# Kernel optimization log

Measured on AMD Instinct MI355X. Metric: run time of the kernel, lower is better.

The kernel has to match this reference:

```python
import jax, jax.numpy as jnp
import numpy as np

NUM_ENTITIES = 500000
NUM_RELATIONS = 1000
NUM_ENTITY_TYPES = 100
NUM_RELATION_TYPES = 50
D = 128
B = 16384


def setup_inputs() -> dict:
    key = jax.random.key(0)
    ks = jax.random.split(key, 9)
    u = lambda k, shape: jax.random.uniform(k, shape, jnp.float32, -0.1, 0.1)
    return {
        "heads": jax.random.randint(ks[0], (B,), 0, NUM_ENTITIES),
        "relations": jax.random.randint(ks[1], (B,), 0, NUM_RELATIONS),
        "tails": jax.random.randint(ks[2], (B,), 0, NUM_ENTITIES),
        "entity_types": jax.random.randint(ks[3], (B,), 0, NUM_ENTITY_TYPES),
        "relation_types": jax.random.randint(ks[4], (B,), 0, NUM_RELATION_TYPES),
        "entity_emb": u(ks[5], (NUM_ENTITIES, D)),
        "relation_emb": u(ks[6], (NUM_RELATIONS, D)),
        "entity_type_proj": u(ks[7], (NUM_ENTITY_TYPES, D * D)),
        "relation_type_proj": u(ks[8], (NUM_RELATION_TYPES, D * D)),
    }


def reference(heads, relations, tails, entity_types, relation_types,
              entity_emb, relation_emb, entity_type_proj, relation_type_proj):
    h = entity_emb[heads]                     # [B, D]
    r = relation_emb[relations]               # [B, D]
    t = entity_emb[tails]                     # [B, D]
    Pe = entity_type_proj[entity_types].reshape(-1, D, D)      # [B, D, D]
    Pr = relation_type_proj[relation_types].reshape(-1, D, D)  # [B, D, D]
    ph = jnp.einsum('bij,bj->bi', Pe, h)
    pt = jnp.einsum('bij,bj->bi', Pe, t)
    pr = jnp.einsum('bij,bj->bi', Pr, r)
    diff = ph + pr - pt                       # [B, D]
    return jnp.linalg.norm(diff, axis=1)      # [B]
```

## Files before the change

kernel.cpp:

```cpp
#include <hip/hip_runtime.h>
#include <math.h>

#define D 128
#define MTILE 32
#define MAXCH 1280
#define NB 1024

#define W_NCH   0
#define W_CHP0  16
#define W_CHN   (16 + MAXCH)
#define W_CHTT  (16 + 2 * MAXCH)
#define W_SRT   4096

__global__ __launch_bounds__(NB) void bucket_kernel(
    const int* __restrict__ etypes, const int* __restrict__ rtypes,
    int* __restrict__ ws, int B)
{
    __shared__ int cnt_e[128], cnt_r[64], off_e[128], off_r[64], tmp[128];
    __shared__ int s_nche;
    const int tid = threadIdx.x;

    if (tid < 128) cnt_e[tid] = 0;
    if (tid < 64)  cnt_r[tid] = 0;
    __syncthreads();
    for (int b = tid; b < B; b += NB) {
        atomicAdd(&cnt_e[etypes[b]], 1);
        atomicAdd(&cnt_r[rtypes[b]], 1);
    }
    __syncthreads();

    int c = (tid < 128) ? cnt_e[tid] : 0;
    if (tid < 128) tmp[tid] = c;
    __syncthreads();
    for (int off = 1; off < 128; off <<= 1) {
        int v = (tid < 128 && tid >= off) ? tmp[tid - off] : 0;
        __syncthreads();
        if (tid < 128) tmp[tid] += v;
        __syncthreads();
    }
    int excl = (tid < 128) ? (tmp[tid] - c) : 0;
    if (tid < 128) off_e[tid] = excl;
    int nch = (tid < 128) ? ((c + MTILE - 1) / MTILE) : 0;
    __syncthreads();
    if (tid < 128) tmp[tid] = nch;
    __syncthreads();
    for (int off = 1; off < 128; off <<= 1) {
        int v = (tid < 128 && tid >= off) ? tmp[tid - off] : 0;
        __syncthreads();
        if (tid < 128) tmp[tid] += v;
        __syncthreads();
    }
    if (tid < 128) {
        int cexcl = tmp[tid] - nch;
        for (int q = 0; q < nch; ++q) {
            int ci = cexcl + q;
            ws[W_CHP0 + ci] = excl + q * MTILE;
            int rem = c - q * MTILE;
            ws[W_CHN + ci] = rem < MTILE ? rem : MTILE;
            ws[W_CHTT + ci] = tid;
        }
    }
    if (tid == 127) s_nche = tmp[127];
    __syncthreads();
    const int NEch = s_nche;

    c = (tid < 64) ? cnt_r[tid] : 0;
    if (tid < 128) tmp[tid] = c;
    __syncthreads();
    for (int off = 1; off < 128; off <<= 1) {
        int v = (tid < 128 && tid >= off) ? tmp[tid - off] : 0;
        __syncthreads();
        if (tid < 128) tmp[tid] += v;
        __syncthreads();
    }
    excl = (tid < 128) ? (tmp[tid] - c) : 0;
    if (tid < 64) off_r[tid] = excl;
    nch = (tid < 64) ? ((c + MTILE - 1) / MTILE) : 0;
    __syncthreads();
    if (tid < 128) tmp[tid] = nch;
    __syncthreads();
    for (int off = 1; off < 128; off <<= 1) {
        int v = (tid < 128 && tid >= off) ? tmp[tid - off] : 0;
        __syncthreads();
        if (tid < 128) tmp[tid] += v;
        __syncthreads();
    }
    if (tid < 64) {
        int cexcl = tmp[tid] - nch;
        for (int q = 0; q < nch; ++q) {
            int ci = NEch + cexcl + q;
            ws[W_CHP0 + ci] = excl + q * MTILE;
            int rem = c - q * MTILE;
            ws[W_CHN + ci] = rem < MTILE ? rem : MTILE;
            ws[W_CHTT + ci] = tid | 256;
        }
    }
    if (tid == 127) ws[W_NCH] = NEch + tmp[127];
    __syncthreads();

    int* srt_e = ws + W_SRT;
    int* inv_e = srt_e + B;
    int* srt_r = inv_e + B;
    int* inv_r = srt_r + B;
    for (int b = tid; b < B; b += NB) {
        int pe = atomicAdd(&off_e[etypes[b]], 1);
        srt_e[pe] = b; inv_e[b] = pe;
        int pr = atomicAdd(&off_r[rtypes[b]], 1);
        srt_r[pr] = b; inv_r[b] = pr;
    }
}

__global__ __launch_bounds__(256) void gemm_fused(
    const int* __restrict__ heads, const int* __restrict__ tails,
    const int* __restrict__ rels,
    const float* __restrict__ eemb, const float* __restrict__ remb,
    const float* __restrict__ eproj, const float* __restrict__ rproj,
    const int* __restrict__ ws, int B,
    float* __restrict__ Ye, float* __restrict__ Yr)
{
    const int nch = ws[W_NCH];
    if ((int)blockIdx.x >= nch) return;
    const int p0  = ws[W_CHP0 + blockIdx.x];
    const int nr  = ws[W_CHN  + blockIdx.x];
    const int tts = ws[W_CHTT + blockIdx.x];
    const int side = tts >> 8, tt = tts & 255;
    const int* srt = ws + W_SRT + (side ? 2 * B : 0);
    const float* P = (side ? rproj : eproj) + (size_t)tt * D * D;
    float* Y = side ? Yr : Ye;

    __shared__ float Xs[MTILE * 132];
    __shared__ float Ps[D * 36];

    const int tid = threadIdx.x;

    for (int idx = tid; idx < MTILE * 32; idx += 256) {
        int row = idx >> 5, kq = idx & 31;
        float4 v = {0.f, 0.f, 0.f, 0.f};
        if (row < nr) {
            int b = srt[p0 + row];
            if (side == 0) {
                float4 hv = ((const float4*)(eemb + (size_t)heads[b] * D))[kq];
                float4 tv = ((const float4*)(eemb + (size_t)tails[b] * D))[kq];
                v.x = hv.x - tv.x; v.y = hv.y - tv.y;
                v.z = hv.z - tv.z; v.w = hv.w - tv.w;
            } else {
                v = ((const float4*)(remb + (size_t)rels[b] * D))[kq];
            }
        }
        *(float4*)&Xs[row * 132 + kq * 4] = v;
    }

    float acc[2][8];
    #pragma unroll
    for (int j = 0; j < 2; ++j)
        #pragma unroll
        for (int i = 0; i < 8; ++i) acc[j][i] = 0.f;

    const int ty = tid >> 4, tx = tid & 15;

    for (int k0 = 0; k0 < 32; k0 += 8) {
        __syncthreads();
        for (int idx = tid; idx < 1024; idx += 256) {
            int n = idx >> 3, kq = idx & 7;
            float4 v = *(const float4*)&P[(size_t)n * D + (k0 + kq) * 4];
            *(float4*)&Ps[n * 36 + kq * 4] = v;
        }
        __syncthreads();

        #pragma unroll
        for (int kq = 0; kq < 8; ++kq) {
            float4 xv[2], pv[8];
            #pragma unroll
            for (int j = 0; j < 2; ++j)
                xv[j] = *(const float4*)&Xs[(ty * 2 + j) * 132 + (k0 + kq) * 4];
            #pragma unroll
            for (int i = 0; i < 8; ++i)
                pv[i] = *(const float4*)&Ps[(i * 16 + tx) * 36 + kq * 4];
            #pragma unroll
            for (int j = 0; j < 2; ++j)
                #pragma unroll
                for (int i = 0; i < 8; ++i)
                    acc[j][i] += xv[j].x * pv[i].x + xv[j].y * pv[i].y
                               + xv[j].z * pv[i].z + xv[j].w * pv[i].w;
        }
    }

    #pragma unroll
    for (int j = 0; j < 2; ++j) {
        int m = ty * 2 + j;
        if (m < nr) {
            float* yp = Y + (size_t)(p0 + m) * D + tx;
            #pragma unroll
            for (int i = 0; i < 8; ++i) yp[i * 16] = acc[j][i];
        }
    }
}

__global__ __launch_bounds__(256) void norm_kernel(
    const int* __restrict__ ws, int B,
    const float* __restrict__ Ye, const float* __restrict__ Yr,
    float* __restrict__ out)
{
    int wave = threadIdx.x >> 6, lane = threadIdx.x & 63;
    int gb = blockIdx.x * 4 + wave;
    if (gb >= B) return;
    int re = ws[W_SRT + B + gb];
    int rr = ws[W_SRT + 3 * B + gb];
    float2 a = ((const float2*)(Ye + (size_t)re * D))[lane];
    float2 c = ((const float2*)(Yr + (size_t)rr * D))[lane];
    float x0 = a.x + c.x, x1 = a.y + c.y;
    float ss = x0 * x0 + x1 * x1;
    #pragma unroll
    for (int off = 32; off > 0; off >>= 1)
        ss += __shfl_down(ss, off, 64);
    if (lane == 0) out[gb] = sqrtf(ss);
}

extern "C" void kernel_launch(void* const* d_in, const int* in_sizes, int n_in,
                              void* d_out, int out_size, void* d_ws, size_t ws_size,
                              hipStream_t stream) {
    const int*   heads     = (const int*)d_in[0];
    const int*   relations = (const int*)d_in[1];
    const int*   tails     = (const int*)d_in[2];
    const int*   etypes    = (const int*)d_in[3];
    const int*   rtypes    = (const int*)d_in[4];
    const float* eemb      = (const float*)d_in[5];
    const float* remb      = (const float*)d_in[6];
    const float* eproj     = (const float*)d_in[7];
    const float* rproj     = (const float*)d_in[8];
    float* out = (float*)d_out;

    const int B = in_sizes[0];
    int* ws = (int*)d_ws;
    float* Ye = (float*)d_ws + (W_SRT + 4 * B);
    float* Yr = Ye + (size_t)B * D;

    bucket_kernel<<<1, NB, 0, stream>>>(etypes, rtypes, ws, B);
    gemm_fused<<<MAXCH, 256, 0, stream>>>(heads, tails, relations,
                                          eemb, remb, eproj, rproj, ws, B, Ye, Yr);
    norm_kernel<<<(B + 3) / 4, 256, 0, stream>>>(ws, B, Ye, Yr, out);
}
```

Measured before the change: 426.8 us.

## Split single-block bucketing into parallel count, scan, and scatter kernels

Replaces the one-block bucket sort with four kernels: zero the counters, count types with a grid-wide global atomic histogram, build offsets and chunk descriptors in one block using a single combined scan plus a binary search per chunk, and scatter indices with a grid-wide pass. This targets the serial cost of one 1024-thread block walking all 16384 items twice. In exchange it adds three kernel launches and contended global atomics on a small number of counters. The scatter order within a type is now nondeterministic across blocks, but the output does not depend on that order.

```diff
diff --git a/kernel.cpp b/kernel.cpp
--- a/kernel.cpp
+++ b/kernel.cpp
@@ -4,32 +4,44 @@
 #define D 128
 #define MTILE 32
 #define MAXCH 1280
-#define NB 1024
 
 #define W_NCH   0
-#define W_CHP0  16
-#define W_CHN   (16 + MAXCH)
-#define W_CHTT  (16 + 2 * MAXCH)
-#define W_SRT   4096
-
-__global__ __launch_bounds__(NB) void bucket_kernel(
+#define W_CNT_E 16
+#define W_CNT_R 144
+#define W_RUN_E 208
+#define W_RUN_R 336
+#define W_CHP0  512
+#define W_CHN   (512 + MAXCH)
+#define W_CHTT  (512 + 2 * MAXCH)
+#define W_SRT   8192
+
+__global__ __launch_bounds__(256) void zero_kernel(int* ws) {
+    int tid = threadIdx.x;
+    if (tid < 192) ws[W_CNT_E + tid] = 0;
+}
+
+__global__ __launch_bounds__(256) void count_kernel(
     const int* __restrict__ etypes, const int* __restrict__ rtypes,
     int* __restrict__ ws, int B)
 {
-    __shared__ int cnt_e[128], cnt_r[64], off_e[128], off_r[64], tmp[128];
-    __shared__ int s_nche;
+    int b = blockIdx.x * blockDim.x + threadIdx.x;
+    if (b < B) {
+        atomicAdd(&ws[W_CNT_E + etypes[b]], 1);
+        atomicAdd(&ws[W_CNT_R + rtypes[b]], 1);
+    }
+}
+
+__global__ __launch_bounds__(256) void scan_build_kernel(int* __restrict__ ws) {
+    __shared__ int s_cnt[192];
+    __shared__ int s_off[192];
+    __shared__ int s_cs[193];
+    __shared__ int tmp[256];
     const int tid = threadIdx.x;
 
-    if (tid < 128) cnt_e[tid] = 0;
-    if (tid < 64)  cnt_r[tid] = 0;
-    __syncthreads();
-    for (int b = tid; b < B; b += NB) {
-        atomicAdd(&cnt_e[etypes[b]], 1);
-        atomicAdd(&cnt_r[rtypes[b]], 1);
-    }
-    __syncthreads();
-
-    int c = (tid < 128) ? cnt_e[tid] : 0;
+    if (tid < 192) s_cnt[tid] = ws[W_CNT_E + tid];
+    __syncthreads();
+
+    int c = (tid < 128) ? s_cnt[tid] : 0;
     if (tid < 128) tmp[tid] = c;
     __syncthreads();
     for (int off = 1; off < 128; off <<= 1) {
@@ -38,74 +50,66 @@
         if (tid < 128) tmp[tid] += v;
         __syncthreads();
     }
-    int excl = (tid < 128) ? (tmp[tid] - c) : 0;
-    if (tid < 128) off_e[tid] = excl;
-    int nch = (tid < 128) ? ((c + MTILE - 1) / MTILE) : 0;
-    __syncthreads();
-    if (tid < 128) tmp[tid] = nch;
-    __syncthreads();
-    for (int off = 1; off < 128; off <<= 1) {
-        int v = (tid < 128 && tid >= off) ? tmp[tid - off] : 0;
-        __syncthreads();
-        if (tid < 128) tmp[tid] += v;
-        __syncthreads();
-    }
-    if (tid < 128) {
-        int cexcl = tmp[tid] - nch;
-        for (int q = 0; q < nch; ++q) {
-            int ci = cexcl + q;
-            ws[W_CHP0 + ci] = excl + q * MTILE;
-            int rem = c - q * MTILE;
-            ws[W_CHN + ci] = rem < MTILE ? rem : MTILE;
-            ws[W_CHTT + ci] = tid;
-        }
-    }
-    if (tid == 127) s_nche = tmp[127];
-    __syncthreads();
-    const int NEch = s_nche;
-
-    c = (tid < 64) ? cnt_r[tid] : 0;
-    if (tid < 128) tmp[tid] = c;
-    __syncthreads();
-    for (int off = 1; off < 128; off <<= 1) {
-        int v = (tid < 128 && tid >= off) ? tmp[tid - off] : 0;
-        __syncthreads();
-        if (tid < 128) tmp[tid] += v;
-        __syncthreads();
-    }
-    excl = (tid < 128) ? (tmp[tid] - c) : 0;
-    if (tid < 64) off_r[tid] = excl;
-    nch = (tid < 64) ? ((c + MTILE - 1) / MTILE) : 0;
-    __syncthreads();
-    if (tid < 128) tmp[tid] = nch;
-    __syncthreads();
-    for (int off = 1; off < 128; off <<= 1) {
-        int v = (tid < 128 && tid >= off) ? tmp[tid - off] : 0;
-        __syncthreads();
-        if (tid < 128) tmp[tid] += v;
-        __syncthreads();
-    }
-    if (tid < 64) {
-        int cexcl = tmp[tid] - nch;
-        for (int q = 0; q < nch; ++q) {
-            int ci = NEch + cexcl + q;
-            ws[W_CHP0 + ci] = excl + q * MTILE;
-            int rem = c - q * MTILE;
-            ws[W_CHN + ci] = rem < MTILE ? rem : MTILE;
-            ws[W_CHTT + ci] = tid | 256;
-        }
-    }
-    if (tid == 127) ws[W_NCH] = NEch + tmp[127];
-    __syncthreads();
-
+    if (tid < 128) s_off[tid] = tmp[tid] - c;
+    __syncthreads();
+
+    c = (tid < 64) ? s_cnt[128 + tid] : 0;
+    if (tid < 64) tmp[tid] = c;
+    __syncthreads();
+    for (int off = 1; off < 64; off <<= 1) {
+        int v = (tid < 64 && tid >= off) ? tmp[tid - off] : 0;
+        __syncthreads();
+        if (tid < 64) tmp[tid] += v;
+        __syncthreads();
+    }
+    if (tid < 64) s_off[128 + tid] = tmp[tid] - c;
+    __syncthreads();
+
+    int nch = (tid < 192) ? ((s_cnt[tid] + MTILE - 1) / MTILE) : 0;
+    tmp[tid] = nch;
+    __syncthreads();
+    for (int off = 1; off < 256; off <<= 1) {
+        int v = (tid >= off) ? tmp[tid - off] : 0;
+        __syncthreads();
+        tmp[tid] += v;
+        __syncthreads();
+    }
+    if (tid < 192) s_cs[tid] = tmp[tid] - nch;
+    if (tid == 191) { s_cs[192] = tmp[191]; ws[W_NCH] = tmp[191]; }
+    __syncthreads();
+
+    if (tid < 192) ws[W_RUN_E + tid] = s_off[tid];
+
+    const int total = s_cs[192];
+    for (int ci = tid; ci < total; ci += 256) {
+        int lo = 0, hi = 192;
+        while (hi - lo > 1) {
+            int mid = (lo + hi) >> 1;
+            if (s_cs[mid] <= ci) lo = mid; else hi = mid;
+        }
+        int q = ci - s_cs[lo];
+        int side = lo >> 7;
+        int type = lo & 127;
+        int rem = s_cnt[lo] - q * MTILE;
+        ws[W_CHP0 + ci] = s_off[lo] + q * MTILE;
+        ws[W_CHN  + ci] = rem < MTILE ? rem : MTILE;
+        ws[W_CHTT + ci] = type | (side << 8);
+    }
+}
+
+__global__ __launch_bounds__(256) void scatter_kernel(
+    const int* __restrict__ etypes, const int* __restrict__ rtypes,
+    int* __restrict__ ws, int B)
+{
     int* srt_e = ws + W_SRT;
     int* inv_e = srt_e + B;
     int* srt_r = inv_e + B;
     int* inv_r = srt_r + B;
-    for (int b = tid; b < B; b += NB) {
-        int pe = atomicAdd(&off_e[etypes[b]], 1);
+    int b = blockIdx.x * blockDim.x + threadIdx.x;
+    if (b < B) {
+        int pe = atomicAdd(&ws[W_RUN_E + etypes[b]], 1);
         srt_e[pe] = b; inv_e[b] = pe;
-        int pr = atomicAdd(&off_r[rtypes[b]], 1);
+        int pr = atomicAdd(&ws[W_RUN_R + rtypes[b]], 1);
         srt_r[pr] = b; inv_r[b] = pr;
     }
 }
@@ -235,7 +239,10 @@
     float* Ye = (float*)d_ws + (W_SRT + 4 * B);
     float* Yr = Ye + (size_t)B * D;
 
-    bucket_kernel<<<1, NB, 0, stream>>>(etypes, rtypes, ws, B);
+    zero_kernel<<<1, 256, 0, stream>>>(ws);
+    count_kernel<<<(B + 255) / 256, 256, 0, stream>>>(etypes, rtypes, ws, B);
+    scan_build_kernel<<<1, 256, 0, stream>>>(ws);
+    scatter_kernel<<<(B + 255) / 256, 256, 0, stream>>>(etypes, rtypes, ws, B);
     gemm_fused<<<MAXCH, 256, 0, stream>>>(heads, tails, relations,
                                           eemb, remb, eproj, rproj, ws, B, Ye, Yr);
     norm_kernel<<<(B + 3) / 4, 256, 0, stream>>>(ws, B, Ye, Yr, out);
```

Result: slower. 455.5 us (+6.7%).
